# Optimization experiments

Measured on AMD Instinct MI355X. Metric: run time of the kernel, lower is better.

The kernel has to match this reference:

```python
import jax, jax.numpy as jnp
import numpy as np

N_NODES = 50000
N_EDGES = 1600000
NODE_DIM = 128
EDGE_DIM = 64
HIDDEN = 128
K_HOPS = 2  # DGL TAGConv default k=2


def _uniform(key, shape, fan_in):
    bound = 1.0 / np.sqrt(fan_in)
    return jax.random.uniform(key, shape, jnp.float32, -bound, bound)


def setup_inputs() -> dict:
    key = jax.random.key(0)
    ks = jax.random.split(key, 12)
    d_msg_in = NODE_DIM + EDGE_DIM
    d_c1_in = (HIDDEN + NODE_DIM) * (K_HOPS + 1)
    d_c2_in = HIDDEN * (K_HOPS + 1)
    return {
        "node_fea": jax.random.normal(ks[0], (N_NODES, NODE_DIM), jnp.float32),
        "edge_fea": jax.random.normal(ks[1], (N_EDGES, EDGE_DIM), jnp.float32),
        "src": jax.random.randint(ks[2], (N_EDGES,), 0, N_NODES),
        "dst": jax.random.randint(ks[3], (N_EDGES,), 0, N_NODES),
        "msg_W": _uniform(ks[4], (d_msg_in, HIDDEN), d_msg_in),
        "msg_b": _uniform(ks[5], (HIDDEN,), d_msg_in),
        "W1": _uniform(ks[6], (d_c1_in, HIDDEN), d_c1_in),
        "b1": _uniform(ks[7], (HIDDEN,), d_c1_in),
        "W2": _uniform(ks[8], (d_c2_in, HIDDEN), d_c2_in),
        "b2": _uniform(ks[9], (HIDDEN,), d_c2_in),
        "Wp": _uniform(ks[10], (HIDDEN, 1), HIDDEN),
        "bp": _uniform(ks[11], (1,), HIDDEN),
    }


def reference(node_fea, edge_fea, src, dst, msg_W, msg_b, W1, b1, W2, b2, Wp, bp):
    n = node_fea.shape[0]
    # --- edge message: relu(Linear([src_fea, edge_fea])) then scatter-sum to dst ---
    msg = jax.nn.relu(jnp.concatenate([node_fea[src], edge_fea], axis=1) @ msg_W + msg_b)
    h_neigh = jax.ops.segment_sum(msg, dst, num_segments=n)  # [N, H]

    # --- TAGConv (k=2) symmetric in-degree normalization, DGL-style ---
    deg = jax.ops.segment_sum(jnp.ones((dst.shape[0],), node_fea.dtype), dst, num_segments=n)
    norm = jnp.maximum(deg, 1.0) ** -0.5  # [N]

    def prop(x):  # x: [N, D] -> norm * A^T (norm * x)
        return norm[:, None] * jax.ops.segment_sum((x * norm[:, None])[src], dst, num_segments=n)

    def tagconv(x, W, b):
        h1 = prop(x)
        h2 = prop(h1)
        return jnp.concatenate([x, h1, h2], axis=1) @ W + b

    h = jax.nn.relu(tagconv(jnp.concatenate([node_fea, h_neigh], axis=1), W1, b1))
    h = jax.nn.relu(tagconv(h, W2, b2))

    # --- dgl.mean_nodes (single graph) then predict ---
    hg = jnp.mean(h, axis=0)  # [H]
    return hg @ Wp + bp  # [1]
```

## Files before the change

### kernel.cpp

```cpp
#include <hip/hip_runtime.h>
#include <hip/hip_bf16.h>


typedef __attribute__((ext_vector_type(8))) short short8;
typedef __attribute__((ext_vector_type(4))) float f32x4;
typedef __attribute__((ext_vector_type(4))) unsigned u32x4;
typedef unsigned short ushort_t;
typedef unsigned char uchar_t;

static __device__ __forceinline__ unsigned short f2bf(float x) {
  union { float f; unsigned u; } v{x};
  unsigned r = v.u + 0x7FFF + ((v.u >> 16) & 1);
  return (unsigned short)(r >> 16);
}
static __device__ __forceinline__ float bf2f(unsigned short h) {
  union { unsigned u; float f; } v{(unsigned)h << 16};
  return v.f;
}
static __device__ __forceinline__ float u2f(unsigned u) {
  union { unsigned u; float f; } v{u};
  return v.f;
}
static __device__ __forceinline__ unsigned cvtpk(float a, float b) {
  unsigned r;
  asm("v_cvt_pk_bf16_f32 %0, %1, %2" : "=v"(r) : "v"(a), "v"(b));
  return r;
}
static __device__ __forceinline__ uchar_t f2fp8(float x) {
  return (uchar_t)(__builtin_amdgcn_cvt_pk_fp8_f32(x, 0.f, 0, false) & 0xff);
}
static __device__ __forceinline__ ushort_t pk2fp8(float a, float b) {
  return (ushort_t)(__builtin_amdgcn_cvt_pk_fp8_f32(a, b, 0, false) & 0xffff);
}

__global__ void k_init(const int* __restrict__ dst, int* __restrict__ deg, int E,
                       const float* __restrict__ msg_W, const float* __restrict__ W1,
                       const float* __restrict__ W2, ushort_t* __restrict__ WfT,
                       ushort_t* __restrict__ WfB, ushort_t* __restrict__ Wf1,
                       ushort_t* __restrict__ Wf2) {
  if (blockIdx.x < 1024) {
    int i = blockIdx.x * 256 + threadIdx.x;
    int stride = 1024 * 256;
    for (; i < E; i += stride) atomicAdd(&deg[dst[i]], 1);
    return;
  }
  int id = (blockIdx.x - 1024) * 256 + threadIdx.x;
  const float* W;
  ushort_t* dh;
  int lid;
  if (id < 16384) {
    W = msg_W; dh = WfT; lid = id;
  } else if (id < 24576) {
    W = msg_W + 128 * 128; dh = WfB; lid = id - 16384;
  } else if (id < 122880) {
    int sub = id - 24576;
    int s = sub >> 15;
    lid = sub & 32767;
    W = W1 + (size_t)s * 256 * 128;
    dh = Wf1 + (size_t)s * 32768;
  } else if (id < 172032) {
    int sub = id - 122880;
    int s = sub >> 14;
    lid = sub & 16383;
    W = W2 + (size_t)s * 128 * 128;
    dh = Wf2 + (size_t)s * 16384;
  } else {
    return;
  }
  int j = lid & 7;
  int l = (lid >> 3) & 63;
  int rest = lid >> 9;
  int ks = rest & 1, nt = (rest >> 1) & 7, kc = rest >> 4;
  int k = kc * 64 + ks * 32 + (l >> 4) * 8 + j;
  int col = nt * 16 + (l & 15);
  dh[lid] = f2bf(W[(size_t)k * 128 + col]);
}

__global__ void k_csr(const int* __restrict__ src, const int* __restrict__ dst,
                      int* __restrict__ cursor, int* __restrict__ csr_srcnode,
                      int* __restrict__ csr_eid, int* __restrict__ pos2node, int E) {
  int i = blockIdx.x * blockDim.x + threadIdx.x;
  int stride = gridDim.x * blockDim.x;
  for (; i < E; i += stride) {
    int d = dst[i];
    int pos = atomicAdd(&cursor[d], 1);
    csr_srcnode[pos] = src[i];
    csr_eid[pos] = i;
    pos2node[pos] = d;
  }
}

static __device__ __forceinline__ void stage_hi(const float* base, int sq, int sr,
                                                ushort_t* Xh) {
#pragma unroll
  for (int i2 = 0; i2 < 2; ++i2) {
    const int o = sq * 2 + i2;
    f32x4 a4 = *(const f32x4*)(base + sq * 16 + i2 * 8);
    f32x4 b4 = *(const f32x4*)(base + sq * 16 + i2 * 8 + 4);
    u32x4 vh;
    vh[0] = cvtpk(a4[0], a4[1]);
    vh[1] = cvtpk(a4[2], a4[3]);
    vh[2] = cvtpk(b4[0], b4[1]);
    vh[3] = cvtpk(b4[2], b4[3]);
    const int slot = (sr >> 4) * 128 + o * 16 + (sr & 15);
    *(u32x4*)(Xh + (size_t)slot * 8) = vh;
  }
}

__global__ __launch_bounds__(256) void k_scan_mmz(
    const int* __restrict__ deg, float* __restrict__ norm, int* __restrict__ offs,
    int* __restrict__ cursor, int N, const float* __restrict__ A0,
    const ushort_t* __restrict__ Wf, const float* __restrict__ bias,
    uchar_t* __restrict__ outZ8, int KC) {
  __shared__ __align__(16) char lds[24576];
  if (blockIdx.x == 0) {
    int* part = (int*)lds;
    const int t = threadIdx.x;
    const int C = (N + 255) >> 8;
    const int b = t * C, e = min(b + C, N);
    int s = 0;
    for (int i = b; i < e; ++i) s += deg[i];
    part[t] = s;
    __syncthreads();
    for (int ofs = 1; ofs < 256; ofs <<= 1) {
      int v = (t >= ofs) ? part[t - ofs] : 0;
      __syncthreads();
      part[t] += v;
      __syncthreads();
    }
    int base = (t == 0) ? 0 : part[t - 1];
    for (int i = b; i < e; ++i) {
      offs[i] = base;
      cursor[i] = base;
      int d = deg[i];
      base += d;
      norm[i] = rsqrtf((float)max(d, 1));
    }
    if (t == 0) offs[N] = part[255];
    return;
  }
  ushort_t* Xh = (ushort_t*)lds;
  ushort_t* Whi = (ushort_t*)(lds + 8192);
  const int t = threadIdx.x;
  const int m0 = (blockIdx.x - 1) * 64;
  const int l = t & 63, mt = t >> 6;
  const int sr = t & 63, sq = t >> 6;
  const int row = min(m0 + sr, N - 1);

  f32x4 acc[8];
#pragma unroll
  for (int nt = 0; nt < 8; ++nt) acc[nt] = (f32x4){0.f, 0.f, 0.f, 0.f};

  for (int kc = 0; kc < KC; ++kc) {
    __syncthreads();
    {
      const ulong2* gh = (const ulong2*)(Wf + (size_t)kc * 8192);
#pragma unroll
      for (int i = 0; i < 4; ++i) ((ulong2*)Whi)[i * 256 + t] = gh[i * 256 + t];
    }
    stage_hi(A0 + (size_t)row * 128 + kc * 64, sq, sr, Xh);
    __syncthreads();
    const short8* Xh8 = (const short8*)Xh;
    const short8* Wh8 = (const short8*)Whi;
#pragma unroll
    for (int ks = 0; ks < 2; ++ks) {
      short8 ah = Xh8[mt * 128 + ks * 64 + l];
#pragma unroll
      for (int nt = 0; nt < 8; ++nt)
        acc[nt] = __builtin_amdgcn_mfma_f32_16x16x32_bf16(
            ah, Wh8[(nt * 2 + ks) * 64 + l], acc[nt], 0, 0, 0);
    }
  }
  const int l15 = l & 15, lh = l >> 4;
#pragma unroll
  for (int nt = 0; nt < 8; ++nt) {
    const int col = nt * 16 + l15;
#pragma unroll
    for (int rg = 0; rg < 4; ++rg) {
      const int r = m0 + mt * 16 + lh * 4 + rg;
      if (r < N) outZ8[(size_t)r * 128 + col] = f2fp8(acc[nt][rg] + bias[col]);
    }
  }
}

template <int BF16A>
__global__ __launch_bounds__(256) void k_mm3(
    const void* __restrict__ A0v, const float* __restrict__ A1, int split64,
    const ushort_t* __restrict__ Wf, const float* __restrict__ rowscale,
    ushort_t* __restrict__ outYA, ushort_t* __restrict__ outYB,
    uchar_t* __restrict__ outYC8, int M, int KC) {
  __shared__ __align__(16) char lds[24576];
  ushort_t* Xh = (ushort_t*)lds;
  ushort_t* Whi = (ushort_t*)(lds + 8192);

  const int t = threadIdx.x;
  const int m0 = blockIdx.x * 64;
  const int l = t & 63, mt = t >> 6;
  const int sr = t & 63, sq = t >> 6;
  const int row = min(m0 + sr, M - 1);

  f32x4 acc[3][8];
#pragma unroll
  for (int s = 0; s < 3; ++s)
#pragma unroll
    for (int nt = 0; nt < 8; ++nt) acc[s][nt] = (f32x4){0.f, 0.f, 0.f, 0.f};

  for (int kc = 0; kc < KC; ++kc) {
    __syncthreads();
    if constexpr (BF16A) {
      const ushort_t* base = (const ushort_t*)A0v + (size_t)row * 128 + kc * 64;
#pragma unroll
      for (int i2 = 0; i2 < 2; ++i2) {
        const int o = sq * 2 + i2;
        short8 v = *(const short8*)(base + sq * 16 + i2 * 8);
        const int slot = (sr >> 4) * 128 + o * 16 + (sr & 15);
        *(short8*)(Xh + (size_t)slot * 8) = v;
      }
    } else {
      const float* A0 = (const float*)A0v;
      const float* base = (kc < split64) ? (A0 + (size_t)row * 128 + kc * 64)
                                         : (A1 + (size_t)row * 128 + (kc - split64) * 64);
      stage_hi(base, sq, sr, Xh);
    }
#pragma unroll
    for (int s = 0; s < 3; ++s) {
      if (s) __syncthreads();
      {
        const ulong2* gh = (const ulong2*)(Wf + ((size_t)s * KC + kc) * 8192);
#pragma unroll
        for (int i = 0; i < 4; ++i) ((ulong2*)Whi)[i * 256 + t] = gh[i * 256 + t];
      }
      __syncthreads();
      const short8* Xh8 = (const short8*)Xh;
      const short8* Wh8 = (const short8*)Whi;
#pragma unroll
      for (int ks = 0; ks < 2; ++ks) {
        short8 ah = Xh8[mt * 128 + ks * 64 + l];
#pragma unroll
        for (int nt = 0; nt < 8; ++nt)
          acc[s][nt] = __builtin_amdgcn_mfma_f32_16x16x32_bf16(
              ah, Wh8[(nt * 2 + ks) * 64 + l], acc[s][nt], 0, 0, 0);
      }
    }
  }
  const int l15 = l & 15, lh = l >> 4;
#pragma unroll
  for (int rg = 0; rg < 4; ++rg) {
    const int r = m0 + mt * 16 + lh * 4 + rg;
    if (r < M) {
      const float rs = rowscale[r];
#pragma unroll
      for (int nt = 0; nt < 8; ++nt) {
        const int col = nt * 16 + l15;
        outYA[(size_t)r * 128 + col] = f2bf(acc[0][nt][rg]);
        outYB[(size_t)r * 128 + col] = f2bf(acc[1][nt][rg] * rs);
        outYC8[(size_t)r * 128 + col] = f2fp8(acc[2][nt][rg] * rs);
      }
    }
  }
}

__global__ __launch_bounds__(1024, 8) void k_edge(
    const float* __restrict__ ef, const int* __restrict__ csr_srcnode,
    const int* __restrict__ csr_eid, const int* __restrict__ pos2node,
    const ushort_t* __restrict__ WfB, const uchar_t* __restrict__ Z8,
    float* __restrict__ h_neigh) {
  __shared__ __align__(16) char lds[33280];
  ushort_t* Xh = (ushort_t*)lds;
  ushort_t* Whi = (ushort_t*)(lds + 16384);
  ushort_t* Cs = (ushort_t*)lds;
  int* sN = (int*)(lds + 32768);

  const int t = threadIdx.x;
  const int b0 = blockIdx.x * 128;
  const int l = t & 63, w = t >> 6;
  const int mt = w >> 1, nh = w & 1;
  const int col = t & 127, g = t >> 7;
  const int rbase = b0 + g * 16;

  uchar_t z8[16];
#pragma unroll
  for (int i = 0; i < 16; ++i)
    z8[i] = Z8[(size_t)csr_srcnode[rbase + i] * 128 + col];
  ((ulong2*)Whi)[t] = ((const ulong2*)WfB)[t];
  {
    const int row = t >> 3, part = t & 7;
    const int eid = csr_eid[b0 + row];
    const float* rowp = ef + (size_t)eid * 64 + part * 8;
    f32x4 a4 = __builtin_nontemporal_load((const f32x4*)rowp);
    f32x4 b4 = __builtin_nontemporal_load((const f32x4*)(rowp + 4));
    u32x4 vh;
    vh[0] = cvtpk(a4[0], a4[1]);
    vh[1] = cvtpk(a4[2], a4[3]);
    vh[2] = cvtpk(b4[0], b4[1]);
    vh[3] = cvtpk(b4[2], b4[3]);
    const int slot = (row >> 4) * 128 + part * 16 + (row & 15);
    *(u32x4*)(Xh + (size_t)slot * 8) = vh;
  }
  __syncthreads();

  f32x4 acc[4];
#pragma unroll
  for (int nt = 0; nt < 4; ++nt) acc[nt] = (f32x4){0.f, 0.f, 0.f, 0.f};
  {
    const short8* Xh8 = (const short8*)Xh;
    const short8* Wh8 = (const short8*)Whi;
#pragma unroll
    for (int ks = 0; ks < 2; ++ks) {
      short8 ah = Xh8[mt * 128 + ks * 64 + l];
#pragma unroll
      for (int nt = 0; nt < 4; ++nt) {
        const int ntg = nh * 4 + nt;
        acc[nt] = __builtin_amdgcn_mfma_f32_16x16x32_bf16(
            ah, Wh8[(ntg * 2 + ks) * 64 + l], acc[nt], 0, 0, 0);
      }
    }
  }
  __syncthreads();
  if (t < 128) sN[t] = pos2node[b0 + t];
  const int l15 = l & 15, lh = l >> 4;
#pragma unroll
  for (int nt = 0; nt < 4; ++nt) {
#pragma unroll
    for (int rg = 0; rg < 4; ++rg) {
      const int row = mt * 16 + lh * 4 + rg;
      const int c = nh * 64 + nt * 16 + l15;
      Cs[row * 128 + (c ^ (((row >> 2) & 3) << 4))] = f2bf(acc[nt][rg]);
    }
  }
  __syncthreads();
  {
    int node = sN[g * 16];
    float ssum = 0.f;
#pragma unroll
    for (int r = 0; r < 16; ++r) {
      const int rr = g * 16 + r;
      float cz = bf2f(Cs[rr * 128 + (col ^ (((rr >> 2) & 3) << 4))]);
      float zf = __builtin_amdgcn_cvt_f32_fp8((int)z8[r], 0);
      float v = fmaxf(cz + zf, 0.f);
      if (r == 0) {
        ssum = v;
      } else {
        int n2 = sN[rr];
        if (n2 == node) {
          ssum += v;
        } else {
          unsafeAtomicAdd(&h_neigh[(size_t)node * 128 + col], ssum);
          node = n2;
          ssum = v;
        }
      }
    }
    unsafeAtomicAdd(&h_neigh[(size_t)node * 128 + col], ssum);
  }
}

__global__ __launch_bounds__(256) void k_propA(
    const uchar_t* __restrict__ YC8, const ushort_t* __restrict__ YBt,
    const int* __restrict__ offs, const int* __restrict__ csr_src,
    const float* __restrict__ norm, uchar_t* __restrict__ Qt8, int N) {
  const int v = blockIdx.x * 4 + (threadIdx.x >> 6);
  const int lane = threadIdx.x & 63;
  if (v >= N) return;
  const int b = offs[v], e = offs[v + 1];
  const ushort_t* yc = (const ushort_t*)YC8;
  float ax0 = 0.f, ay0 = 0.f, ax1 = 0.f, ay1 = 0.f;
  float ax2 = 0.f, ay2 = 0.f, ax3 = 0.f, ay3 = 0.f;
  int i = b;
  const int e4 = b + ((e - b) & ~3);
  for (; i < e4; i += 4) {
    const int s0 = csr_src[i], s1 = csr_src[i + 1];
    const int s2 = csr_src[i + 2], s3 = csr_src[i + 3];
    const int x0 = yc[(size_t)s0 * 64 + lane];
    const int x1 = yc[(size_t)s1 * 64 + lane];
    const int x2 = yc[(size_t)s2 * 64 + lane];
    const int x3 = yc[(size_t)s3 * 64 + lane];
    auto d0 = __builtin_amdgcn_cvt_pk_f32_fp8(x0, false);
    auto d1 = __builtin_amdgcn_cvt_pk_f32_fp8(x1, false);
    auto d2 = __builtin_amdgcn_cvt_pk_f32_fp8(x2, false);
    auto d3 = __builtin_amdgcn_cvt_pk_f32_fp8(x3, false);
    ax0 += d0[0]; ay0 += d0[1];
    ax1 += d1[0]; ay1 += d1[1];
    ax2 += d2[0]; ay2 += d2[1];
    ax3 += d3[0]; ay3 += d3[1];
  }
  for (; i < e; ++i) {
    const int x = yc[(size_t)csr_src[i] * 64 + lane];
    auto d = __builtin_amdgcn_cvt_pk_f32_fp8(x, false);
    ax0 += d[0]; ay0 += d[1];
  }
  const float ax = (ax0 + ax1) + (ax2 + ax3);
  const float ay = (ay0 + ay1) + (ay2 + ay3);
  const float n = norm[v];
  const float n2 = n * n;
  const unsigned yb = ((const unsigned*)YBt)[(size_t)v * 64 + lane];
  ((ushort_t*)Qt8)[(size_t)v * 64 + lane] =
      pk2fp8(u2f(yb << 16) + n2 * ax, u2f(yb & 0xffff0000u) + n2 * ay);
}

__global__ __launch_bounds__(256) void k_propB(
    const uchar_t* __restrict__ Qt8, const ushort_t* __restrict__ YAb,
    const float* __restrict__ bias, const int* __restrict__ offs,
    const int* __restrict__ csr_src, const float* __restrict__ norm,
    ushort_t* __restrict__ H, int N) {
  const int v = blockIdx.x * 4 + (threadIdx.x >> 6);
  const int lane = threadIdx.x & 63;
  if (v >= N) return;
  const int b = offs[v], e = offs[v + 1];
  const ushort_t* qp = (const ushort_t*)Qt8;
  float ax0 = 0.f, ay0 = 0.f, ax1 = 0.f, ay1 = 0.f;
  float ax2 = 0.f, ay2 = 0.f, ax3 = 0.f, ay3 = 0.f;
  int i = b;
  const int e4 = b + ((e - b) & ~3);
  for (; i < e4; i += 4) {
    const int s0 = csr_src[i], s1 = csr_src[i + 1];
    const int s2 = csr_src[i + 2], s3 = csr_src[i + 3];
    const int x0 = qp[(size_t)s0 * 64 + lane];
    const int x1 = qp[(size_t)s1 * 64 + lane];
    const int x2 = qp[(size_t)s2 * 64 + lane];
    const int x3 = qp[(size_t)s3 * 64 + lane];
    auto d0 = __builtin_amdgcn_cvt_pk_f32_fp8(x0, false);
    auto d1 = __builtin_amdgcn_cvt_pk_f32_fp8(x1, false);
    auto d2 = __builtin_amdgcn_cvt_pk_f32_fp8(x2, false);
    auto d3 = __builtin_amdgcn_cvt_pk_f32_fp8(x3, false);
    ax0 += d0[0]; ay0 += d0[1];
    ax1 += d1[0]; ay1 += d1[1];
    ax2 += d2[0]; ay2 += d2[1];
    ax3 += d3[0]; ay3 += d3[1];
  }
  for (; i < e; ++i) {
    const int x = qp[(size_t)csr_src[i] * 64 + lane];
    auto d = __builtin_amdgcn_cvt_pk_f32_fp8(x, false);
    ax0 += d[0]; ay0 += d[1];
  }
  const float ax = (ax0 + ax1) + (ax2 + ax3);
  const float ay = (ay0 + ay1) + (ay2 + ay3);
  const float n = norm[v];
  const unsigned ya = ((const unsigned*)YAb)[(size_t)v * 64 + lane];
  const float2 bb = ((const float2*)bias)[lane];
  const float hx = fmaxf(u2f(ya << 16) + n * ax + bb.x, 0.f);
  const float hy = fmaxf(u2f(ya & 0xffff0000u) + n * ay + bb.y, 0.f);
  ((unsigned*)H)[(size_t)v * 64 + lane] = cvtpk(hx, hy);
}

__global__ void k_colsum(const ushort_t* __restrict__ h, float* __restrict__ hg, int N) {
  const int t = threadIdx.x;
  const int per = (N + gridDim.x - 1) / gridDim.x;
  const int n0 = blockIdx.x * per, n1 = min(n0 + per, N);
  float s = 0.f;
  for (int n = n0; n < n1; ++n) s += bf2f(h[(size_t)n * 128 + t]);
  unsafeAtomicAdd(&hg[t], s);
}

__global__ void k_final(const float* __restrict__ hg, const float* __restrict__ Wp,
                        const float* __restrict__ bp, float* __restrict__ out,
                        float invN) {
  __shared__ float red[128];
  const int t = threadIdx.x;
  red[t] = hg[t] * invN * Wp[t];
  __syncthreads();
  for (int s = 64; s > 0; s >>= 1) {
    if (t < s) red[t] += red[t + s];
    __syncthreads();
  }
  if (t == 0) out[0] = red[0] + bp[0];
}

extern "C" void kernel_launch(void* const* d_in, const int* in_sizes, int n_in,
                              void* d_out, int out_size, void* d_ws, size_t ws_size,
                              hipStream_t stream) {
  const float* node_fea = (const float*)d_in[0];
  const float* edge_fea = (const float*)d_in[1];
  const int* src = (const int*)d_in[2];
  const int* dst = (const int*)d_in[3];
  const float* msg_W = (const float*)d_in[4];
  const float* msg_b = (const float*)d_in[5];
  const float* W1 = (const float*)d_in[6];
  const float* b1 = (const float*)d_in[7];
  const float* W2 = (const float*)d_in[8];
  const float* b2 = (const float*)d_in[9];
  const float* Wp = (const float*)d_in[10];
  const float* bp = (const float*)d_in[11];

  const int N = in_sizes[0] / 128;
  const int E = in_sizes[2];

  char* p = (char*)d_ws;
  auto alloc = [&](size_t bytes) {
    char* r = p;
    p += (bytes + 255) & ~(size_t)255;
    return r;
  };
  int* deg = (int*)alloc((size_t)N * 4);
  float* norm = (float*)alloc((size_t)N * 4);
  int* offs = (int*)alloc((size_t)(N + 1) * 4);
  int* cursor = (int*)alloc((size_t)N * 4);
  int* csr_srcnode = (int*)alloc((size_t)E * 4);
  int* csr_eid = (int*)alloc((size_t)E * 4);
  int* pos2node = (int*)alloc((size_t)E * 4);
  ushort_t* WfT = (ushort_t*)alloc(2 * 8192 * 2);
  ushort_t* WfB = (ushort_t*)alloc(1 * 8192 * 2);
  ushort_t* Wf1 = (ushort_t*)alloc(3 * 4 * 8192 * 2);
  ushort_t* Wf2 = (ushort_t*)alloc(3 * 2 * 8192 * 2);
  uchar_t* Z8 = (uchar_t*)alloc((size_t)N * 128);
  ushort_t* YAb = (ushort_t*)alloc((size_t)N * 128 * 2);
  float* hn = (float*)alloc((size_t)N * 128 * 4);
  ushort_t* YBt = (ushort_t*)alloc((size_t)N * 128 * 2);
  uchar_t* YC8 = (uchar_t*)alloc((size_t)N * 128);
  uchar_t* Qt8 = (uchar_t*)alloc((size_t)N * 128);
  ushort_t* H1 = (ushort_t*)alloc((size_t)N * 128 * 2);
  ushort_t* H2 = (ushort_t*)alloc((size_t)N * 128 * 2);
  float* hg = (float*)alloc(128 * 4);

  (void)hipMemsetAsync(deg, 0, (size_t)N * 4, stream);
  (void)hipMemsetAsync(hn, 0, (size_t)N * 128 * 4, stream);
  (void)hipMemsetAsync(hg, 0, 128 * 4, stream);

  k_init<<<1696, 256, 0, stream>>>(dst, deg, E, msg_W, W1, W2, WfT, WfB, Wf1, Wf2);

  const int MB = (N + 63) / 64;
  const int PB = (N + 3) / 4;

  k_scan_mmz<<<MB + 1, 256, 0, stream>>>(deg, norm, offs, cursor, N, node_fea,
                                         WfT, msg_b, Z8, 2);
  k_csr<<<2048, 256, 0, stream>>>(src, dst, cursor, csr_srcnode, csr_eid, pos2node, E);
  k_edge<<<E / 128, 1024, 0, stream>>>(edge_fea, csr_srcnode, csr_eid, pos2node,
                                       WfB, Z8, hn);

  k_mm3<0><<<MB, 256, 0, stream>>>(node_fea, hn, 2, Wf1, norm, YAb, YBt, YC8, N, 4);
  k_propA<<<PB, 256, 0, stream>>>(YC8, YBt, offs, csr_srcnode, norm, Qt8, N);
  k_propB<<<PB, 256, 0, stream>>>(Qt8, YAb, b1, offs, csr_srcnode, norm, H1, N);

  k_mm3<1><<<MB, 256, 0, stream>>>(H1, nullptr, 0, Wf2, norm, YAb, YBt, YC8, N, 2);
  k_propA<<<PB, 256, 0, stream>>>(YC8, YBt, offs, csr_srcnode, norm, Qt8, N);
  k_propB<<<PB, 256, 0, stream>>>(Qt8, YAb, b2, offs, csr_srcnode, norm, H2, N);

  k_colsum<<<256, 128, 0, stream>>>(H2, hg, N);
  k_final<<<1, 128, 0, stream>>>(hg, Wp, bp, (float*)d_out, 1.0f / (float)N);
}
```

Before: 833.6 us.

## Make edge kernel persistent with software-prefetched gathers of next tile

Turns k_edge into a persistent grid-stride kernel with 512 blocks, so the weight tile is loaded into LDS once per block rather than once per 128-edge tile. While the current tile is being processed, it prefetches the next tile's FP8 Z gathers and edge ids into registers, overlapping gather latency with MFMA and atomic work. LDS is enlarged so that Xh/Cs no longer alias the weights, and launch bounds are relaxed to 4 blocks per CU. This raises register and LDS use and adds an extra barrier per tile, which may lower occupancy.

```diff
diff --git a/kernel.cpp b/kernel.cpp
--- a/kernel.cpp
+++ b/kernel.cpp
@@ -260,98 +260,121 @@
   }
 }
 
-__global__ __launch_bounds__(1024, 8) void k_edge(
+__global__ __launch_bounds__(1024, 4) void k_edge(
     const float* __restrict__ ef, const int* __restrict__ csr_srcnode,
     const int* __restrict__ csr_eid, const int* __restrict__ pos2node,
     const ushort_t* __restrict__ WfB, const uchar_t* __restrict__ Z8,
-    float* __restrict__ h_neigh) {
-  __shared__ __align__(16) char lds[33280];
-  ushort_t* Xh = (ushort_t*)lds;
-  ushort_t* Whi = (ushort_t*)(lds + 16384);
-  ushort_t* Cs = (ushort_t*)lds;
-  int* sN = (int*)(lds + 32768);
+    float* __restrict__ h_neigh, int nT) {
+  __shared__ __align__(16) char lds[49664];
+  ushort_t* Whi = (ushort_t*)lds;
+  ushort_t* Xh = (ushort_t*)(lds + 16384);
+  ushort_t* Cs = (ushort_t*)(lds + 16384);
+  int* sN = (int*)(lds + 49152);
 
   const int t = threadIdx.x;
-  const int b0 = blockIdx.x * 128;
   const int l = t & 63, w = t >> 6;
   const int mt = w >> 1, nh = w & 1;
   const int col = t & 127, g = t >> 7;
-  const int rbase = b0 + g * 16;
-
+  const int erow = t >> 3, epart = t & 7;
+  const int l15 = l & 15, lh = l >> 4;
+
+  ((ulong2*)Whi)[t] = ((const ulong2*)WfB)[t];
+
+  int tile = blockIdx.x;
   uchar_t z8[16];
-#pragma unroll
-  for (int i = 0; i < 16; ++i)
-    z8[i] = Z8[(size_t)csr_srcnode[rbase + i] * 128 + col];
-  ((ulong2*)Whi)[t] = ((const ulong2*)WfB)[t];
-  {
-    const int row = t >> 3, part = t & 7;
-    const int eid = csr_eid[b0 + row];
-    const float* rowp = ef + (size_t)eid * 64 + part * 8;
-    f32x4 a4 = __builtin_nontemporal_load((const f32x4*)rowp);
-    f32x4 b4 = __builtin_nontemporal_load((const f32x4*)(rowp + 4));
-    u32x4 vh;
-    vh[0] = cvtpk(a4[0], a4[1]);
-    vh[1] = cvtpk(a4[2], a4[3]);
-    vh[2] = cvtpk(b4[0], b4[1]);
-    vh[3] = cvtpk(b4[2], b4[3]);
-    const int slot = (row >> 4) * 128 + part * 16 + (row & 15);
-    *(u32x4*)(Xh + (size_t)slot * 8) = vh;
-  }
-  __syncthreads();
-
-  f32x4 acc[4];
-#pragma unroll
-  for (int nt = 0; nt < 4; ++nt) acc[nt] = (f32x4){0.f, 0.f, 0.f, 0.f};
-  {
-    const short8* Xh8 = (const short8*)Xh;
-    const short8* Wh8 = (const short8*)Whi;
-#pragma unroll
-    for (int ks = 0; ks < 2; ++ks) {
-      short8 ah = Xh8[mt * 128 + ks * 64 + l];
-#pragma unroll
-      for (int nt = 0; nt < 4; ++nt) {
-        const int ntg = nh * 4 + nt;
-        acc[nt] = __builtin_amdgcn_mfma_f32_16x16x32_bf16(
-            ah, Wh8[(ntg * 2 + ks) * 64 + l], acc[nt], 0, 0, 0);
-      }
-    }
-  }
-  __syncthreads();
-  if (t < 128) sN[t] = pos2node[b0 + t];
-  const int l15 = l & 15, lh = l >> 4;
-#pragma unroll
-  for (int nt = 0; nt < 4; ++nt) {
-#pragma unroll
-    for (int rg = 0; rg < 4; ++rg) {
-      const int row = mt * 16 + lh * 4 + rg;
-      const int c = nh * 64 + nt * 16 + l15;
-      Cs[row * 128 + (c ^ (((row >> 2) & 3) << 4))] = f2bf(acc[nt][rg]);
-    }
-  }
-  __syncthreads();
-  {
-    int node = sN[g * 16];
-    float ssum = 0.f;
-#pragma unroll
-    for (int r = 0; r < 16; ++r) {
-      const int rr = g * 16 + r;
-      float cz = bf2f(Cs[rr * 128 + (col ^ (((rr >> 2) & 3) << 4))]);
-      float zf = __builtin_amdgcn_cvt_f32_fp8((int)z8[r], 0);
-      float v = fmaxf(cz + zf, 0.f);
-      if (r == 0) {
-        ssum = v;
-      } else {
-        int n2 = sN[rr];
-        if (n2 == node) {
-          ssum += v;
+  int eid = 0;
+  if (tile < nT) {
+    const int b0 = tile * 128;
+#pragma unroll
+    for (int i = 0; i < 16; ++i)
+      z8[i] = Z8[(size_t)csr_srcnode[b0 + g * 16 + i] * 128 + col];
+    eid = csr_eid[b0 + erow];
+  }
+
+  for (; tile < nT; tile += gridDim.x) {
+    const int b0 = tile * 128;
+    {
+      const float* rowp = ef + (size_t)eid * 64 + epart * 8;
+      f32x4 a4 = __builtin_nontemporal_load((const f32x4*)rowp);
+      f32x4 b4 = __builtin_nontemporal_load((const f32x4*)(rowp + 4));
+      u32x4 vh;
+      vh[0] = cvtpk(a4[0], a4[1]);
+      vh[1] = cvtpk(a4[2], a4[3]);
+      vh[2] = cvtpk(b4[0], b4[1]);
+      vh[3] = cvtpk(b4[2], b4[3]);
+      const int slot = (erow >> 4) * 128 + epart * 16 + (erow & 15);
+      *(u32x4*)(Xh + (size_t)slot * 8) = vh;
+      if (t < 128) sN[t] = pos2node[b0 + t];
+    }
+    uchar_t z8n[16];
+    int eidn = 0;
+    {
+      const int ntile = tile + gridDim.x;
+      if (ntile < nT) {
+        const int nb0 = ntile * 128;
+#pragma unroll
+        for (int i = 0; i < 16; ++i)
+          z8n[i] = Z8[(size_t)csr_srcnode[nb0 + g * 16 + i] * 128 + col];
+        eidn = csr_eid[nb0 + erow];
+      }
+    }
+    __syncthreads();
+    f32x4 acc[4];
+#pragma unroll
+    for (int nt = 0; nt < 4; ++nt) acc[nt] = (f32x4){0.f, 0.f, 0.f, 0.f};
+    {
+      const short8* Xh8 = (const short8*)Xh;
+      const short8* Wh8 = (const short8*)Whi;
+#pragma unroll
+      for (int ks = 0; ks < 2; ++ks) {
+        short8 ah = Xh8[mt * 128 + ks * 64 + l];
+#pragma unroll
+        for (int nt = 0; nt < 4; ++nt) {
+          const int ntg = nh * 4 + nt;
+          acc[nt] = __builtin_amdgcn_mfma_f32_16x16x32_bf16(
+              ah, Wh8[(ntg * 2 + ks) * 64 + l], acc[nt], 0, 0, 0);
+        }
+      }
+    }
+    __syncthreads();
+#pragma unroll
+    for (int nt = 0; nt < 4; ++nt) {
+#pragma unroll
+      for (int rg = 0; rg < 4; ++rg) {
+        const int row = mt * 16 + lh * 4 + rg;
+        const int c = nh * 64 + nt * 16 + l15;
+        Cs[row * 128 + (c ^ (((row >> 2) & 3) << 4))] = f2bf(acc[nt][rg]);
+      }
+    }
+    __syncthreads();
+    {
+      int node = sN[g * 16];
+      float ssum = 0.f;
+#pragma unroll
+      for (int r = 0; r < 16; ++r) {
+        const int rr = g * 16 + r;
+        float cz = bf2f(Cs[rr * 128 + (col ^ (((rr >> 2) & 3) << 4))]);
+        float zf = __builtin_amdgcn_cvt_f32_fp8((int)z8[r], 0);
+        float v = fmaxf(cz + zf, 0.f);
+        if (r == 0) {
+          ssum = v;
         } else {
-          unsafeAtomicAdd(&h_neigh[(size_t)node * 128 + col], ssum);
-          node = n2;
-          ssum = v;
+          int n2 = sN[rr];
+          if (n2 == node) {
+            ssum += v;
+          } else {
+            unsafeAtomicAdd(&h_neigh[(size_t)node * 128 + col], ssum);
+            node = n2;
+            ssum = v;
+          }
         }
       }
-    }
-    unsafeAtomicAdd(&h_neigh[(size_t)node * 128 + col], ssum);
+      unsafeAtomicAdd(&h_neigh[(size_t)node * 128 + col], ssum);
+    }
+#pragma unroll
+    for (int i = 0; i < 16; ++i) z8[i] = z8n[i];
+    eid = eidn;
+    __syncthreads();
   }
 }
 
@@ -524,8 +547,8 @@
   k_scan_mmz<<<MB + 1, 256, 0, stream>>>(deg, norm, offs, cursor, N, node_fea,
                                          WfT, msg_b, Z8, 2);
   k_csr<<<2048, 256, 0, stream>>>(src, dst, cursor, csr_srcnode, csr_eid, pos2node, E);
-  k_edge<<<E / 128, 1024, 0, stream>>>(edge_fea, csr_srcnode, csr_eid, pos2node,
-                                       WfB, Z8, hn);
+  k_edge<<<512, 1024, 0, stream>>>(edge_fea, csr_srcnode, csr_eid, pos2node,
+                                   WfB, Z8, hn, E / 128);
 
   k_mm3<0><<<MB, 256, 0, stream>>>(node_fea, hn, 2, Wf1, norm, YAb, YBt, YC8, N, 4);
   k_propA<<<PB, 256, 0, stream>>>(YC8, YBt, offs, csr_srcnode, norm, Qt8, N);
```

Result: slower. 908.7 us (+9.0%).
